# Performance work log

Hardware: AMD Instinct MI355X
Metric: run time of the kernel (lower is better)

The kernel has to match this reference:

```python
import jax, jax.numpy as jnp
import numpy as np

N, D, H1, K = 4096, 128, 256, 128


def setup_inputs() -> dict:
    key = jax.random.key(0)
    ks = jax.random.split(key, 8)
    A = jax.random.uniform(ks[3], (D, D), dtype=jnp.float32)
    A = A * (1.0 - jnp.eye(D, dtype=jnp.float32))  # DAG prob mask, no self-loops
    return {
        "x": jax.random.normal(ks[0], (N, D), dtype=jnp.float32),
        "weight": jax.random.normal(ks[1], (D, D), dtype=jnp.float32) * 0.1,
        "bias": jax.random.normal(ks[2], (1, D), dtype=jnp.float32) * 0.1,
        "A": A,
        "W1": jax.random.normal(ks[4], (D, H1), dtype=jnp.float32) * 0.1,
        "b1": jax.random.normal(ks[5], (H1,), dtype=jnp.float32) * 0.1,
        "W2": jax.random.normal(ks[6], (H1, K), dtype=jnp.float32) * 0.1,
        "b2": jax.random.normal(ks[7], (K,), dtype=jnp.float32) * 0.1,
    }


def reference(x, weight, bias, A, W1, b1, W2, b2):
    # to_adj (eval path): masked weights
    W = weight * A                                   # [D, D]
    y = x @ W + bias                                 # [N, D]
    # __expand__ builds diag(y[n]) [N,D,D]; since e[n,i,:] = y[n,i]*I[i,:],
    # the first Linear collapses to a per-row scaling of W1 (same math, fused):
    # e @ W1 -> y[n,i] * W1[i,:]
    h1 = jax.nn.relu(y[:, :, None] * W1[None, :, :] + b1)   # [N, D, H1]
    f = (h1 @ W2 + b2).sum(axis=2)                   # [N, D] (sum over output dim)
    # h_func, method='gnn'
    I = jnp.eye(D, dtype=x.dtype)
    A2 = jnp.square(W)
    M = I + A2 / D
    E = jnp.linalg.matrix_power(M, D - 1)
    h_val = (E.T * M).sum() - D
    # l1_reg (same prob mask in eval)
    reg = jnp.abs(W).sum()
    return (f, h_val, reg)
```

## Files before the change

### kernel.cpp

```cpp
#include <hip/hip_runtime.h>

#define NN 4096
#define DD 128
#define HH1 256

#define WS_S    0
#define WS_S2   16384
#define WS_S3   32768
#define WS_S4   49152
#define WS_W    65536
#define WS_W2S  81920
#define WS_PAIR 82176
#define WS_B2S  82688
#define WS_TACC 82696
#define WS_DONE 82708
#define WS_REGP 82712
#define WS_XT   82944
#define WS_REQ_FLOATS 607232
#define WS_REQ_BYTES  (WS_REQ_FLOATS * 4UL)

#define O_S    0
#define O_S2   16384
#define O_S3   32768
#define O_S4   49152
#define O_W2S  65536
#define O_B2S  65792
#define O_TACC 65808
#define O_DONE 65824
#define O_REGP 65840

__device__ __forceinline__ float waveReduce(float v) {
#pragma unroll
  for (int off = 32; off > 0; off >>= 1) v += __shfl_down(v, off, 64);
  return v;
}


__global__ __launch_bounds__(256) void kA2(
    const float* __restrict__ weight, const float* __restrict__ Amat,
    const float* __restrict__ W2, const float* __restrict__ b2,
    const float* __restrict__ b1v, const float* __restrict__ x,
    float* __restrict__ ws) {
  const int b = blockIdx.x, tid = threadIdx.x;
  __shared__ float s_lds[DD * DD];
  __shared__ float xs[128 * 133];
  if (b < 64) {
    const float4* w4 = (const float4*)weight;
    const float4* a4 = (const float4*)Amat;
    float4* s4 = (float4*)s_lds;
    const float inv = 1.0f / 128.0f;
    for (int e = tid; e < DD * DD / 4; e += 256) {
      float4 wv = w4[e], av = a4[e], o;
      float t;
      t = wv.x * av.x; o.x = t * t * inv;
      t = wv.y * av.y; o.y = t * t * inv;
      t = wv.z * av.z; o.z = t * t * inv;
      t = wv.w * av.w; o.w = t * t * inv;
      s4[e] = o;
    }
    __syncthreads();
    const int i = (b << 1) + (tid >> 7), j = tid & 127;
    const float* row = &s_lds[i * DD];
    float acc = 0.f;
#pragma unroll 8
    for (int k = 0; k < DD; ++k) acc = fmaf(row[k], s_lds[k * DD + j], acc);
    ws[WS_S2 + i * DD + j] = acc;
  } else if (b < 72) {
    const int base = (b - 64) * 2048;
    const float inv = 1.0f / 128.0f;
    for (int e = tid; e < 2048; e += 256) {
      const int idx = base + e;
      const float w = weight[idx] * Amat[idx];
      ws[WS_W + idx] = w;
      ws[WS_S + idx] = w * w * inv;
    }
  } else if (b == 72) {
    const float4* r = (const float4*)(W2 + tid * 128);
    float4 s4 = make_float4(0.f, 0.f, 0.f, 0.f);
#pragma unroll 8
    for (int k = 0; k < 32; ++k) {
      const float4 v = r[k];
      s4.x += v.x; s4.y += v.y; s4.z += v.z; s4.w += v.w;
    }
    const float w2sv = (s4.x + s4.y) + (s4.z + s4.w);
    ws[WS_W2S + tid] = w2sv;
    ((float2*)(ws + WS_PAIR))[tid] = make_float2(b1v[tid], w2sv);
  } else if (b == 73) {
    __shared__ float red[4];
    float v = (tid < 128) ? b2[tid] : 0.f;
    v = waveReduce(v);
    if ((tid & 63) == 0) red[tid >> 6] = v;
    __syncthreads();
    if (tid == 0) ws[WS_B2S] = (red[0] + red[1]) + (red[2] + red[3]);
    if (tid >= 64 && tid < 74) ws[WS_TACC + (tid - 64)] = 0.f;
    if (tid == 96) *(unsigned int*)(ws + WS_DONE) = 0u;
  } else if (b < 82) {
    const int bb = b - 74;
    const int base = bb * 2048;
    float s = 0.f;
    for (int e = tid; e < 2048; e += 256) {
      const int idx = base + e;
      s += fabsf(weight[idx] * Amat[idx]);
    }
    s = waveReduce(s);
    __shared__ float red2[4];
    if ((tid & 63) == 0) red2[tid >> 6] = s;
    __syncthreads();
    if (tid == 0) ws[WS_REGP + bb] = (red2[0] + red2[1]) + (red2[2] + red2[3]);
  } else {
    const int n0 = (b - 82) * 128;
    const float4* x4 = (const float4*)x;
    for (int e = tid; e < 4096; e += 256) {
      const int r = e >> 5, c = e & 31;
      const float4 v = x4[(n0 + r) * 32 + c];
      float* p = &xs[r * 133 + (c << 2)];
      p[0] = v.x; p[1] = v.y; p[2] = v.z; p[3] = v.w;
    }
    __syncthreads();
    float* xT = ws + WS_XT;
    const int c = tid & 31, ks = tid >> 5;
#pragma unroll 4
    for (int m = 0; m < 16; ++m) {
      const int k = ks + (m << 3);
      float4 o;
      o.x = xs[((c << 2) + 0) * 133 + k];
      o.y = xs[((c << 2) + 1) * 133 + k];
      o.z = xs[((c << 2) + 2) * 133 + k];
      o.w = xs[((c << 2) + 3) * 133 + k];
      *(float4*)&xT[k * NN + n0 + (c << 2)] = o;
    }
  }
}

__global__ __launch_bounds__(512) void kB3(const float* __restrict__ bias,
                                           const float* __restrict__ W1,
                                           float* __restrict__ ws,
                                           float* __restrict__ out) {
  const int tid = threadIdx.x;
  if (blockIdx.x < 64) {
    const int sb = blockIdx.x;
    const bool isS4 = sb >= 32;
    const int mb = isS4 ? sb - 32 : sb;
    const float* __restrict__ L = ws + WS_S2;
    const float* __restrict__ R = ws + (isS4 ? WS_S2 : WS_S);
    float* __restrict__ O = ws + (isS4 ? WS_S4 : WS_S3);
    const int i = (mb << 2) + (tid >> 7), j = tid & 127;
    float acc = 0.f;
#pragma unroll 8
    for (int k = 0; k < DD; ++k) acc = fmaf(L[i * DD + k], R[k * DD + j], acc);
    O[i * DD + j] = acc;
    return;
  }
  const int fb = blockIdx.x - 64;
  const int n0 = (fb & 15) << 8;
  const int i0 = (fb >> 4) << 3;
  const int w = tid >> 6, l = tid & 63;
  __shared__ float xs[32][256];
  __shared__ float ts[256][9];
  const float* __restrict__ xT = ws + WS_XT;
  const float* __restrict__ Wm = ws + WS_W;
  const int iu = __builtin_amdgcn_readfirstlane(i0 + w);

  float t[4] = {0.f, 0.f, 0.f, 0.f};
  for (int kc = 0; kc < 4; ++kc) {
    __syncthreads();
    {
      const float4* src = (const float4*)(xT + (kc * 32) * NN + n0);
      float4* dst4 = (float4*)&xs[0][0];
#pragma unroll
      for (int m = 0; m < 4; ++m) {
        const int e = tid + (m << 9);
        const int kk = e >> 6, c = e & 63;
        dst4[(kk << 6) + c] = src[kk * (NN / 4) + c];
      }
    }
    __syncthreads();
#pragma unroll
    for (int kk = 0; kk < 32; ++kk) {
      const float wv = Wm[(kc * 32 + kk) * DD + iu];
      const float4 xv = *(const float4*)&xs[kk][l << 2];
      t[0] = fmaf(xv.x, wv, t[0]);
      t[1] = fmaf(xv.y, wv, t[1]);
      t[2] = fmaf(xv.z, wv, t[2]);
      t[3] = fmaf(xv.w, wv, t[3]);
    }
  }
  const float bv = bias[iu];
#pragma unroll
  for (int q = 0; q < 4; ++q) t[q] += bv;

  const float sb2 = ws[WS_B2S];
  float acc[4];
#pragma unroll
  for (int q = 0; q < 4; ++q) acc[q] = sb2;
  const float* __restrict__ W1row = W1 + iu * HH1;
  const float2* __restrict__ pr = (const float2*)(ws + WS_PAIR);
#pragma unroll 8
  for (int j = 0; j < HH1; ++j) {
    const float sw1 = W1row[j];
    const float2 p = pr[j];
    const float vb = p.x;
#pragma unroll
    for (int q = 0; q < 4; ++q) {
      const float h = fmaxf(fmaf(t[q], sw1, vb), 0.f);
      acc[q] = fmaf(h, p.y, acc[q]);
    }
  }
#pragma unroll
  for (int q = 0; q < 4; ++q) ts[(l << 2) + q][w] = acc[q];
  __syncthreads();
  {
    const int m = tid >> 1, half = tid & 1;
    float4 o;
    o.x = ts[m][(half << 2) + 0];
    o.y = ts[m][(half << 2) + 1];
    o.z = ts[m][(half << 2) + 2];
    o.w = ts[m][(half << 2) + 3];
    *(float4*)&out[(n0 + m) * DD + i0 + (half << 2)] = o;
  }
}

__global__ __launch_bounds__(256) void kC3(float* __restrict__ ws,
                                           float* __restrict__ out) {
  const int tid = threadIdx.x;
  const int tb = blockIdx.x;
  const int i = (tb << 1) + (tid >> 7), j = tid & 127;
  const float* S1 = ws + WS_S;
  const float* S2 = ws + WS_S2;
  const float* S3 = ws + WS_S3;
  const float* S4 = ws + WS_S4;
  const float a1 = S1[i * DD + j], a2 = S2[i * DD + j], a3 = S3[i * DD + j];
  const float b1t = S1[j * DD + i], b2t = S2[j * DD + i],
              b3t = S3[j * DD + i], b4t = S4[j * DD + i];
  float e7 = 0.f;
#pragma unroll 8
  for (int k = 0; k < DD; ++k) e7 = fmaf(S3[i * DD + k], S4[k * DD + j], e7);
  float c[10];
  c[0] = a1 * b1t; c[1] = a2 * b1t; c[2] = a2 * b2t; c[3] = a3 * b2t;
  c[4] = a3 * b3t; c[5] = a3 * b4t; c[6] = e7 * b1t; c[7] = e7 * b2t;
  c[8] = e7 * b3t; c[9] = e7 * b4t;
  __shared__ float red[4][10];
#pragma unroll
  for (int m = 0; m < 10; ++m) {
    const float v = waveReduce(c[m]);
    if ((tid & 63) == 0) red[tid >> 6][m] = v;
  }
  __syncthreads();
  if (tid == 0) {
    float* tacc = ws + WS_TACC;
    for (int m = 0; m < 10; ++m)
      atomicAdd(&tacc[m], (red[0][m] + red[1][m]) + (red[2][m] + red[3][m]));
    __threadfence();
    unsigned int* done = (unsigned int*)(ws + WS_DONE);
    const unsigned int old = atomicAdd(done, 1u);
    if (old == 63u) {
      __threadfence();
      double h = 0.0, C = 8128.0;
      for (int kk = 2; kk <= 11; ++kk) {
        const float tv = atomicAdd(&tacc[kk - 2], 0.0f);
        h += C * (double)tv;
        C = C * (double)(128 - kk) / (double)(kk + 1);
      }
      float reg = 0.f;
      for (int m = 0; m < 8; ++m) reg += ws[WS_REGP + m];
      out[NN * DD] = (float)h;
      out[NN * DD + 1] = reg;
    }
  }
}

__global__ __launch_bounds__(256) void kA_old(
    const float* __restrict__ weight, const float* __restrict__ Amat,
    const float* __restrict__ W2, const float* __restrict__ b2,
    float* __restrict__ ws) {
  const int b = blockIdx.x, tid = threadIdx.x;
  if (b < 64) {
    __shared__ float s_lds[DD * DD];
    const float4* w4 = (const float4*)weight;
    const float4* a4 = (const float4*)Amat;
    float4* s4 = (float4*)s_lds;
    const float inv = 1.0f / 128.0f;
    for (int e = tid; e < DD * DD / 4; e += 256) {
      float4 wv = w4[e], av = a4[e], o;
      float t;
      t = wv.x * av.x; o.x = t * t * inv;
      t = wv.y * av.y; o.y = t * t * inv;
      t = wv.z * av.z; o.z = t * t * inv;
      t = wv.w * av.w; o.w = t * t * inv;
      s4[e] = o;
    }
    __syncthreads();
    const int i = (b << 1) + (tid >> 7), j = tid & 127;
    const float* row = &s_lds[i * DD];
    float acc = 0.f;
#pragma unroll 8
    for (int k = 0; k < DD; ++k) acc = fmaf(row[k], s_lds[k * DD + j], acc);
    ws[O_S2 + i * DD + j] = acc;
  } else if (b < 72) {
    const int base = (b - 64) * 2048;
    const float inv = 1.0f / 128.0f;
    for (int e = tid; e < 2048; e += 256) {
      const int idx = base + e;
      const float w = weight[idx] * Amat[idx];
      ws[O_S + idx] = w * w * inv;
    }
  } else if (b == 72) {
    const float4* r = (const float4*)(W2 + tid * 128);
    float4 s4 = make_float4(0.f, 0.f, 0.f, 0.f);
#pragma unroll 8
    for (int k = 0; k < 32; ++k) {
      const float4 v = r[k];
      s4.x += v.x; s4.y += v.y; s4.z += v.z; s4.w += v.w;
    }
    ws[O_W2S + tid] = (s4.x + s4.y) + (s4.z + s4.w);
  } else if (b == 73) {
    __shared__ float red[4];
    float v = (tid < 128) ? b2[tid] : 0.f;
    v = waveReduce(v);
    if ((tid & 63) == 0) red[tid >> 6] = v;
    __syncthreads();
    if (tid == 0) ws[O_B2S] = (red[0] + red[1]) + (red[2] + red[3]);
    if (tid >= 64 && tid < 74) ws[O_TACC + (tid - 64)] = 0.f;
    if (tid == 96) *(unsigned int*)(ws + O_DONE) = 0u;
  } else {
    const int bb = b - 74;
    const int base = bb * 2048;
    float s = 0.f;
    for (int e = tid; e < 2048; e += 256) {
      const int idx = base + e;
      s += fabsf(weight[idx] * Amat[idx]);
    }
    s = waveReduce(s);
    __shared__ float red[4];
    if ((tid & 63) == 0) red[tid >> 6] = s;
    __syncthreads();
    if (tid == 0) ws[O_REGP + bb] = (red[0] + red[1]) + (red[2] + red[3]);
  }
}

__global__ __launch_bounds__(256) void kB_old(
    const float* __restrict__ x, const float* __restrict__ weight,
    const float* __restrict__ Amat, const float* __restrict__ bias,
    const float* __restrict__ W1, const float* __restrict__ b1v,
    float* __restrict__ ws, float* __restrict__ out) {
  const int tid = threadIdx.x;
  if (blockIdx.x < 128) {
    const int sb = blockIdx.x;
    const bool isS4 = sb >= 64;
    const int mb = isS4 ? sb - 64 : sb;
    const float* __restrict__ L = ws + O_S2;
    const float* __restrict__ R = ws + (isS4 ? O_S2 : O_S);
    float* __restrict__ O = ws + (isS4 ? O_S4 : O_S3);
    const int i = (mb << 1) + (tid >> 7), j = tid & 127;
    float acc = 0.f;
#pragma unroll 8
    for (int k = 0; k < DD; ++k) acc = fmaf(L[i * DD + k], R[k * DD + j], acc);
    O[i * DD + j] = acc;
    return;
  }
  __shared__ float xs[64 * 132];
  __shared__ float4 fq[4 * 256];
  __shared__ float wcol[4 * 128];
  __shared__ float ts[64 * 5];
  const int fb = blockIdx.x - 128;
  const int i0 = (fb & 31) << 2, n0 = (fb >> 5) << 6;
  const float4* x4 = (const float4*)x;
  for (int e = tid; e < 64 * 32; e += 256) {
    const int r = e >> 5, c = e & 31;
    *(float4*)&xs[r * 132 + (c << 2)] = x4[(n0 + r) * 32 + c];
  }
  for (int e = tid; e < 512; e += 256) {
    const int w = e >> 7, k = e & 127;
    const int gi = k * DD + i0 + w;
    wcol[(w << 7) + k] = weight[gi] * Amat[gi];
  }
  const float* w2s = ws + O_W2S;
  for (int e = tid; e < 1024; e += 256) {
    const int w = e >> 8, j = e & 255;
    fq[(w << 8) + j] = make_float4(W1[(i0 + w) * HH1 + j], b1v[j], w2s[j], 0.f);
  }
  __syncthreads();
  const int w = tid >> 6, l = tid & 63;
  float t = bias[i0 + w];
  const float4* xr = (const float4*)&xs[l * 132];
  const float4* wc = (const float4*)&wcol[w << 7];
#pragma unroll
  for (int k = 0; k < 32; ++k) {
    const float4 xv = xr[k], wv = wc[k];
    t = fmaf(xv.x, wv.x, t);
    t = fmaf(xv.y, wv.y, t);
    t = fmaf(xv.z, wv.z, t);
    t = fmaf(xv.w, wv.w, t);
  }
  float acc = ws[O_B2S];
  const float4* fp = &fq[w << 8];
#pragma unroll 8
  for (int j = 0; j < HH1; ++j) {
    const float4 c = fp[j];
    acc = fmaf(fmaxf(fmaf(t, c.x, c.y), 0.f), c.z, acc);
  }
  ts[l * 5 + w] = acc;
  __syncthreads();
  if (tid < 64) {
    const float4 o = make_float4(ts[tid * 5 + 0], ts[tid * 5 + 1],
                                 ts[tid * 5 + 2], ts[tid * 5 + 3]);
    *(float4*)&out[(n0 + tid) * DD + i0] = o;
  }
}

__global__ __launch_bounds__(256) void kC_old(float* __restrict__ ws,
                                              float* __restrict__ out) {
  const int tid = threadIdx.x;
  const int i = (blockIdx.x << 1) + (tid >> 7), j = tid & 127;
  const float* S1 = ws + O_S;
  const float* S2 = ws + O_S2;
  const float* S3 = ws + O_S3;
  const float* S4 = ws + O_S4;
  const float a1 = S1[i * DD + j], a2 = S2[i * DD + j], a3 = S3[i * DD + j];
  const float b1t = S1[j * DD + i], b2t = S2[j * DD + i],
              b3t = S3[j * DD + i], b4t = S4[j * DD + i];
  float e7 = 0.f;
#pragma unroll 8
  for (int k = 0; k < DD; ++k) e7 = fmaf(S3[i * DD + k], S4[k * DD + j], e7);
  float c[10];
  c[0] = a1 * b1t; c[1] = a2 * b1t; c[2] = a2 * b2t; c[3] = a3 * b2t;
  c[4] = a3 * b3t; c[5] = a3 * b4t; c[6] = e7 * b1t; c[7] = e7 * b2t;
  c[8] = e7 * b3t; c[9] = e7 * b4t;
  __shared__ float red[4][10];
#pragma unroll
  for (int m = 0; m < 10; ++m) {
    const float v = waveReduce(c[m]);
    if ((tid & 63) == 0) red[tid >> 6][m] = v;
  }
  __syncthreads();
  if (tid == 0) {
    float* tacc = ws + O_TACC;
    for (int m = 0; m < 10; ++m)
      atomicAdd(&tacc[m], (red[0][m] + red[1][m]) + (red[2][m] + red[3][m]));
    __threadfence();
    unsigned int* done = (unsigned int*)(ws + O_DONE);
    const unsigned int old = atomicAdd(done, 1u);
    if (old == 63u) {
      __threadfence();
      double h = 0.0, C = 8128.0;
      for (int kk = 2; kk <= 11; ++kk) {
        const float tv = atomicAdd(&tacc[kk - 2], 0.0f);
        h += C * (double)tv;
        C = C * (double)(128 - kk) / (double)(kk + 1);
      }
      float reg = 0.f;
      for (int m = 0; m < 8; ++m) reg += ws[O_REGP + m];
      out[NN * DD] = (float)h;
      out[NN * DD + 1] = reg;
    }
  }
}

extern "C" void kernel_launch(void* const* d_in, const int* in_sizes, int n_in,
                              void* d_out, int out_size, void* d_ws,
                              size_t ws_size, hipStream_t stream) {
  const float* x      = (const float*)d_in[0];
  const float* weight = (const float*)d_in[1];
  const float* bias   = (const float*)d_in[2];
  const float* Amat   = (const float*)d_in[3];
  const float* W1     = (const float*)d_in[4];
  const float* b1v    = (const float*)d_in[5];
  const float* W2     = (const float*)d_in[6];
  const float* b2     = (const float*)d_in[7];
  float* out = (float*)d_out;
  float* ws  = (float*)d_ws;

  if (ws_size >= WS_REQ_BYTES) {
    kA2<<<114, 256, 0, stream>>>(weight, Amat, W2, b2, b1v, x, ws);
    kB3<<<320, 512, 0, stream>>>(bias, W1, ws, out);
    kC3<<<64, 256, 0, stream>>>(ws, out);
  } else {
    kA_old<<<82, 256, 0, stream>>>(weight, Amat, W2, b2, ws);
    kB_old<<<128 + 2048, 256, 0, stream>>>(x, weight, Amat, bias, W1, b1v, ws,
                                           out);
    kC_old<<<64, 256, 0, stream>>>(ws, out);
  }
}
```

Before: 116.3 us.

## Fuse three kernels into one persistent kernel with software grid barriers

```diff
diff --git a/kernel.cpp b/kernel.cpp
--- a/kernel.cpp
+++ b/kernel.cpp
@@ -15,8 +15,10 @@
 #define WS_TACC 82696
 #define WS_DONE 82708
 #define WS_REGP 82712
-#define WS_XT   82944
-#define WS_REQ_FLOATS 607232
+#define WS_BAR  82720
+#define WS_WT   82944
+#define WS_XT   99328
+#define WS_REQ_FLOATS 623616
 #define WS_REQ_BYTES  (WS_REQ_FLOATS * 4UL)
 
 #define O_S    0
@@ -35,21 +37,40 @@
   return v;
 }
 
-
-__global__ __launch_bounds__(256) void kA2(
-    const float* __restrict__ weight, const float* __restrict__ Amat,
+__device__ __forceinline__ void gridBarrier(unsigned int* bar,
+                                            unsigned int nblk) {
+  __syncthreads();
+  if (threadIdx.x == 0) {
+    __threadfence();
+    __hip_atomic_fetch_add(bar, 1u, __ATOMIC_ACQ_REL,
+                           __HIP_MEMORY_SCOPE_AGENT);
+    unsigned int v = __hip_atomic_load(bar, __ATOMIC_ACQUIRE,
+                                       __HIP_MEMORY_SCOPE_AGENT);
+    while (v < nblk) {
+      __builtin_amdgcn_s_sleep(2);
+      v = __hip_atomic_load(bar, __ATOMIC_ACQUIRE,
+                            __HIP_MEMORY_SCOPE_AGENT);
+    }
+  }
+  __syncthreads();
+}
+
+__global__ __launch_bounds__(512) void kFused(
+    const float* __restrict__ x, const float* __restrict__ weight,
+    const float* __restrict__ Amat, const float* __restrict__ bias,
+    const float* __restrict__ W1, const float* __restrict__ b1v,
     const float* __restrict__ W2, const float* __restrict__ b2,
-    const float* __restrict__ b1v, const float* __restrict__ x,
-    float* __restrict__ ws) {
+    float* __restrict__ ws, float* __restrict__ out) {
+  __shared__ float smem[17024];
   const int b = blockIdx.x, tid = threadIdx.x;
-  __shared__ float s_lds[DD * DD];
-  __shared__ float xs[128 * 133];
-  if (b < 64) {
+  unsigned int* bar = (unsigned int*)(ws + WS_BAR);
+
+  if (b < 32) {
     const float4* w4 = (const float4*)weight;
     const float4* a4 = (const float4*)Amat;
-    float4* s4 = (float4*)s_lds;
+    float4* s4 = (float4*)smem;
     const float inv = 1.0f / 128.0f;
-    for (int e = tid; e < DD * DD / 4; e += 256) {
+    for (int e = tid; e < DD * DD / 4; e += 512) {
       float4 wv = w4[e], av = a4[e], o;
       float t;
       t = wv.x * av.x; o.x = t * t * inv;
@@ -59,88 +80,165 @@
       s4[e] = o;
     }
     __syncthreads();
-    const int i = (b << 1) + (tid >> 7), j = tid & 127;
-    const float* row = &s_lds[i * DD];
+    const int i = (b << 2) + (tid >> 7), j = tid & 127;
+    const float* row = &smem[i * DD];
     float acc = 0.f;
 #pragma unroll 8
-    for (int k = 0; k < DD; ++k) acc = fmaf(row[k], s_lds[k * DD + j], acc);
+    for (int k = 0; k < DD; ++k) acc = fmaf(row[k], smem[k * DD + j], acc);
     ws[WS_S2 + i * DD + j] = acc;
-  } else if (b < 72) {
-    const int base = (b - 64) * 2048;
+  } else if (b < 40) {
+    const int base = (b - 32) * 2048;
     const float inv = 1.0f / 128.0f;
-    for (int e = tid; e < 2048; e += 256) {
+    for (int e = tid; e < 2048; e += 512) {
       const int idx = base + e;
       const float w = weight[idx] * Amat[idx];
+      const int k = idx >> 7, i = idx & 127;
       ws[WS_W + idx] = w;
+      ws[WS_WT + i * DD + k] = w;
       ws[WS_S + idx] = w * w * inv;
     }
-  } else if (b == 72) {
-    const float4* r = (const float4*)(W2 + tid * 128);
-    float4 s4 = make_float4(0.f, 0.f, 0.f, 0.f);
-#pragma unroll 8
-    for (int k = 0; k < 32; ++k) {
-      const float4 v = r[k];
-      s4.x += v.x; s4.y += v.y; s4.z += v.z; s4.w += v.w;
-    }
-    const float w2sv = (s4.x + s4.y) + (s4.z + s4.w);
-    ws[WS_W2S + tid] = w2sv;
-    ((float2*)(ws + WS_PAIR))[tid] = make_float2(b1v[tid], w2sv);
-  } else if (b == 73) {
-    __shared__ float red[4];
+  } else if (b == 40) {
+    if (tid < 256) {
+      const float4* r = (const float4*)(W2 + tid * 128);
+      float4 s4 = make_float4(0.f, 0.f, 0.f, 0.f);
+#pragma unroll 8
+      for (int k = 0; k < 32; ++k) {
+        const float4 v = r[k];
+        s4.x += v.x; s4.y += v.y; s4.z += v.z; s4.w += v.w;
+      }
+      const float w2sv = (s4.x + s4.y) + (s4.z + s4.w);
+      ws[WS_W2S + tid] = w2sv;
+      ((float2*)(ws + WS_PAIR))[tid] = make_float2(b1v[tid], w2sv);
+    }
+  } else if (b == 41) {
     float v = (tid < 128) ? b2[tid] : 0.f;
     v = waveReduce(v);
+    float* red = smem;
     if ((tid & 63) == 0) red[tid >> 6] = v;
     __syncthreads();
-    if (tid == 0) ws[WS_B2S] = (red[0] + red[1]) + (red[2] + red[3]);
+    if (tid == 0) {
+      float s = 0.f;
+      for (int m = 0; m < 8; ++m) s += red[m];
+      ws[WS_B2S] = s;
+    }
     if (tid >= 64 && tid < 74) ws[WS_TACC + (tid - 64)] = 0.f;
     if (tid == 96) *(unsigned int*)(ws + WS_DONE) = 0u;
-  } else if (b < 82) {
-    const int bb = b - 74;
+  } else if (b < 50) {
+    const int bb = b - 42;
     const int base = bb * 2048;
     float s = 0.f;
-    for (int e = tid; e < 2048; e += 256) {
+    for (int e = tid; e < 2048; e += 512) {
       const int idx = base + e;
       s += fabsf(weight[idx] * Amat[idx]);
     }
     s = waveReduce(s);
-    __shared__ float red2[4];
+    float* red2 = smem;
     if ((tid & 63) == 0) red2[tid >> 6] = s;
     __syncthreads();
-    if (tid == 0) ws[WS_REGP + bb] = (red2[0] + red2[1]) + (red2[2] + red2[3]);
-  } else {
-    const int n0 = (b - 82) * 128;
+    if (tid == 0) {
+      float t = 0.f;
+      for (int m = 0; m < 8; ++m) t += red2[m];
+      ws[WS_REGP + bb] = t;
+    }
+  } else if (b < 82) {
+    const int n0 = (b - 50) * 128;
     const float4* x4 = (const float4*)x;
-    for (int e = tid; e < 4096; e += 256) {
+    for (int e = tid; e < 4096; e += 512) {
       const int r = e >> 5, c = e & 31;
       const float4 v = x4[(n0 + r) * 32 + c];
-      float* p = &xs[r * 133 + (c << 2)];
+      float* p = &smem[r * 133 + (c << 2)];
       p[0] = v.x; p[1] = v.y; p[2] = v.z; p[3] = v.w;
     }
     __syncthreads();
     float* xT = ws + WS_XT;
     const int c = tid & 31, ks = tid >> 5;
-#pragma unroll 4
-    for (int m = 0; m < 16; ++m) {
-      const int k = ks + (m << 3);
+#pragma unroll
+    for (int m = 0; m < 8; ++m) {
+      const int k = ks + (m << 4);
       float4 o;
-      o.x = xs[((c << 2) + 0) * 133 + k];
-      o.y = xs[((c << 2) + 1) * 133 + k];
-      o.z = xs[((c << 2) + 2) * 133 + k];
-      o.w = xs[((c << 2) + 3) * 133 + k];
+      o.x = smem[((c << 2) + 0) * 133 + k];
+      o.y = smem[((c << 2) + 1) * 133 + k];
+      o.z = smem[((c << 2) + 2) * 133 + k];
+      o.w = smem[((c << 2) + 3) * 133 + k];
       *(float4*)&xT[k * NN + n0 + (c << 2)] = o;
     }
   }
-}
-
-__global__ __launch_bounds__(512) void kB3(const float* __restrict__ bias,
-                                           const float* __restrict__ W1,
-                                           float* __restrict__ ws,
-                                           float* __restrict__ out) {
-  const int tid = threadIdx.x;
-  if (blockIdx.x < 64) {
-    const int sb = blockIdx.x;
-    const bool isS4 = sb >= 32;
-    const int mb = isS4 ? sb - 32 : sb;
+
+  gridBarrier(bar, 256);
+
+  {
+    const int fb = b;
+    const int n0 = (fb & 15) << 8, i0 = (fb >> 4) << 3;
+    const int w = tid >> 6, l = tid & 63;
+    float* xs = smem;
+    float* ts = smem + 8192;
+    const float* __restrict__ xT = ws + WS_XT;
+    const float* __restrict__ WTm = ws + WS_WT;
+    const int iu = __builtin_amdgcn_readfirstlane(i0 + w);
+
+    float t[4] = {0.f, 0.f, 0.f, 0.f};
+    for (int kc = 0; kc < 4; ++kc) {
+      __syncthreads();
+      {
+        const float4* src = (const float4*)(xT + (kc * 32) * NN + n0);
+        float4* dst4 = (float4*)xs;
+#pragma unroll
+        for (int m = 0; m < 4; ++m) {
+          const int e = tid + (m << 9);
+          const int kk = e >> 6, c = e & 63;
+          dst4[(kk << 6) + c] = src[kk * (NN / 4) + c];
+        }
+      }
+      __syncthreads();
+      const float* wr = WTm + iu * DD + kc * 32;
+#pragma unroll
+      for (int kk = 0; kk < 32; ++kk) {
+        const float wv = wr[kk];
+        const float4 xv = *(const float4*)&xs[kk * 256 + (l << 2)];
+        t[0] = fmaf(xv.x, wv, t[0]);
+        t[1] = fmaf(xv.y, wv, t[1]);
+        t[2] = fmaf(xv.z, wv, t[2]);
+        t[3] = fmaf(xv.w, wv, t[3]);
+      }
+    }
+    const float bv = bias[iu];
+#pragma unroll
+    for (int q = 0; q < 4; ++q) t[q] += bv;
+
+    const float sb2 = ws[WS_B2S];
+    float acc[4];
+#pragma unroll
+    for (int q = 0; q < 4; ++q) acc[q] = sb2;
+    const float* __restrict__ W1row = W1 + iu * HH1;
+    const float2* __restrict__ pr = (const float2*)(ws + WS_PAIR);
+#pragma unroll 8
+    for (int j = 0; j < HH1; ++j) {
+      const float sw1 = W1row[j];
+      const float2 p = pr[j];
+      const float vb = p.x;
+#pragma unroll
+      for (int q = 0; q < 4; ++q) {
+        const float h = fmaxf(fmaf(t[q], sw1, vb), 0.f);
+        acc[q] = fmaf(h, p.y, acc[q]);
+      }
+    }
+#pragma unroll
+    for (int q = 0; q < 4; ++q) ts[((l << 2) + q) * 9 + w] = acc[q];
+    __syncthreads();
+    {
+      const int m = tid >> 1, half = tid & 1;
+      float4 o;
+      o.x = ts[m * 9 + (half << 2) + 0];
+      o.y = ts[m * 9 + (half << 2) + 1];
+      o.z = ts[m * 9 + (half << 2) + 2];
+      o.w = ts[m * 9 + (half << 2) + 3];
+      *(float4*)&out[(n0 + m) * DD + i0 + (half << 2)] = o;
+    }
+  }
+
+  if (b < 64) {
+    const bool isS4 = b >= 32;
+    const int mb = b & 31;
     const float* __restrict__ L = ws + WS_S2;
     const float* __restrict__ R = ws + (isS4 ? WS_S2 : WS_S);
     float* __restrict__ O = ws + (isS4 ? WS_S4 : WS_S3);
@@ -149,122 +247,58 @@
 #pragma unroll 8
     for (int k = 0; k < DD; ++k) acc = fmaf(L[i * DD + k], R[k * DD + j], acc);
     O[i * DD + j] = acc;
-    return;
-  }
-  const int fb = blockIdx.x - 64;
-  const int n0 = (fb & 15) << 8;
-  const int i0 = (fb >> 4) << 3;
-  const int w = tid >> 6, l = tid & 63;
-  __shared__ float xs[32][256];
-  __shared__ float ts[256][9];
-  const float* __restrict__ xT = ws + WS_XT;
-  const float* __restrict__ Wm = ws + WS_W;
-  const int iu = __builtin_amdgcn_readfirstlane(i0 + w);
-
-  float t[4] = {0.f, 0.f, 0.f, 0.f};
-  for (int kc = 0; kc < 4; ++kc) {
-    __syncthreads();
-    {
-      const float4* src = (const float4*)(xT + (kc * 32) * NN + n0);
-      float4* dst4 = (float4*)&xs[0][0];
-#pragma unroll
-      for (int m = 0; m < 4; ++m) {
-        const int e = tid + (m << 9);
-        const int kk = e >> 6, c = e & 63;
-        dst4[(kk << 6) + c] = src[kk * (NN / 4) + c];
-      }
-    }
-    __syncthreads();
-#pragma unroll
-    for (int kk = 0; kk < 32; ++kk) {
-      const float wv = Wm[(kc * 32 + kk) * DD + iu];
-      const float4 xv = *(const float4*)&xs[kk][l << 2];
-      t[0] = fmaf(xv.x, wv, t[0]);
-      t[1] = fmaf(xv.y, wv, t[1]);
-      t[2] = fmaf(xv.z, wv, t[2]);
-      t[3] = fmaf(xv.w, wv, t[3]);
-    }
-  }
-  const float bv = bias[iu];
-#pragma unroll
-  for (int q = 0; q < 4; ++q) t[q] += bv;
-
-  const float sb2 = ws[WS_B2S];
-  float acc[4];
-#pragma unroll
-  for (int q = 0; q < 4; ++q) acc[q] = sb2;
-  const float* __restrict__ W1row = W1 + iu * HH1;
-  const float2* __restrict__ pr = (const float2*)(ws + WS_PAIR);
-#pragma unroll 8
-  for (int j = 0; j < HH1; ++j) {
-    const float sw1 = W1row[j];
-    const float2 p = pr[j];
-    const float vb = p.x;
-#pragma unroll
-    for (int q = 0; q < 4; ++q) {
-      const float h = fmaxf(fmaf(t[q], sw1, vb), 0.f);
-      acc[q] = fmaf(h, p.y, acc[q]);
-    }
-  }
-#pragma unroll
-  for (int q = 0; q < 4; ++q) ts[(l << 2) + q][w] = acc[q];
-  __syncthreads();
+  }
+
+  gridBarrier(bar + 1, 256);
+
+  if (b >= 32) return;
+
   {
-    const int m = tid >> 1, half = tid & 1;
-    float4 o;
-    o.x = ts[m][(half << 2) + 0];
-    o.y = ts[m][(half << 2) + 1];
-    o.z = ts[m][(half << 2) + 2];
-    o.w = ts[m][(half << 2) + 3];
-    *(float4*)&out[(n0 + m) * DD + i0 + (half << 2)] = o;
-  }
-}
-
-__global__ __launch_bounds__(256) void kC3(float* __restrict__ ws,
-                                           float* __restrict__ out) {
-  const int tid = threadIdx.x;
-  const int tb = blockIdx.x;
-  const int i = (tb << 1) + (tid >> 7), j = tid & 127;
-  const float* S1 = ws + WS_S;
-  const float* S2 = ws + WS_S2;
-  const float* S3 = ws + WS_S3;
-  const float* S4 = ws + WS_S4;
-  const float a1 = S1[i * DD + j], a2 = S2[i * DD + j], a3 = S3[i * DD + j];
-  const float b1t = S1[j * DD + i], b2t = S2[j * DD + i],
-              b3t = S3[j * DD + i], b4t = S4[j * DD + i];
-  float e7 = 0.f;
-#pragma unroll 8
-  for (int k = 0; k < DD; ++k) e7 = fmaf(S3[i * DD + k], S4[k * DD + j], e7);
-  float c[10];
-  c[0] = a1 * b1t; c[1] = a2 * b1t; c[2] = a2 * b2t; c[3] = a3 * b2t;
-  c[4] = a3 * b3t; c[5] = a3 * b4t; c[6] = e7 * b1t; c[7] = e7 * b2t;
-  c[8] = e7 * b3t; c[9] = e7 * b4t;
-  __shared__ float red[4][10];
-#pragma unroll
-  for (int m = 0; m < 10; ++m) {
-    const float v = waveReduce(c[m]);
-    if ((tid & 63) == 0) red[tid >> 6][m] = v;
-  }
-  __syncthreads();
-  if (tid == 0) {
-    float* tacc = ws + WS_TACC;
-    for (int m = 0; m < 10; ++m)
-      atomicAdd(&tacc[m], (red[0][m] + red[1][m]) + (red[2][m] + red[3][m]));
-    __threadfence();
-    unsigned int* done = (unsigned int*)(ws + WS_DONE);
-    const unsigned int old = atomicAdd(done, 1u);
-    if (old == 63u) {
+    const int i = (b << 2) + (tid >> 7), j = tid & 127;
+    const float* S1 = ws + WS_S;
+    const float* S2 = ws + WS_S2;
+    const float* S3 = ws + WS_S3;
+    const float* S4 = ws + WS_S4;
+    const float a1 = S1[i * DD + j], a2 = S2[i * DD + j], a3 = S3[i * DD + j];
+    const float b1t = S1[j * DD + i], b2t = S2[j * DD + i],
+                b3t = S3[j * DD + i], b4t = S4[j * DD + i];
+    float e7 = 0.f;
+#pragma unroll 8
+    for (int k = 0; k < DD; ++k) e7 = fmaf(S3[i * DD + k], S4[k * DD + j], e7);
+    float c[10];
+    c[0] = a1 * b1t; c[1] = a2 * b1t; c[2] = a2 * b2t; c[3] = a3 * b2t;
+    c[4] = a3 * b3t; c[5] = a3 * b4t; c[6] = e7 * b1t; c[7] = e7 * b2t;
+    c[8] = e7 * b3t; c[9] = e7 * b4t;
+    float* red = smem;
+#pragma unroll
+    for (int m = 0; m < 10; ++m) {
+      const float v = waveReduce(c[m]);
+      if ((tid & 63) == 0) red[(tid >> 6) * 10 + m] = v;
+    }
+    __syncthreads();
+    if (tid == 0) {
+      float* tacc = ws + WS_TACC;
+      for (int m = 0; m < 10; ++m) {
+        float s = 0.f;
+        for (int wv = 0; wv < 8; ++wv) s += red[wv * 10 + m];
+        atomicAdd(&tacc[m], s);
+      }
       __threadfence();
-      double h = 0.0, C = 8128.0;
-      for (int kk = 2; kk <= 11; ++kk) {
-        const float tv = atomicAdd(&tacc[kk - 2], 0.0f);
-        h += C * (double)tv;
-        C = C * (double)(128 - kk) / (double)(kk + 1);
-      }
-      float reg = 0.f;
-      for (int m = 0; m < 8; ++m) reg += ws[WS_REGP + m];
-      out[NN * DD] = (float)h;
-      out[NN * DD + 1] = reg;
+      unsigned int* done = (unsigned int*)(ws + WS_DONE);
+      const unsigned int old = atomicAdd(done, 1u);
+      if (old == 31u) {
+        __threadfence();
+        double h = 0.0, C = 8128.0;
+        for (int kk = 2; kk <= 11; ++kk) {
+          const float tv = atomicAdd(&tacc[kk - 2], 0.0f);
+          h += C * (double)tv;
+          C = C * (double)(128 - kk) / (double)(kk + 1);
+        }
+        float reg = 0.f;
+        for (int m = 0; m < 8; ++m) reg += ws[WS_REGP + m];
+        out[NN * DD] = (float)h;
+        out[NN * DD + 1] = reg;
+      }
     }
   }
 }
@@ -471,9 +505,9 @@
   float* ws  = (float*)d_ws;
 
   if (ws_size >= WS_REQ_BYTES) {
-    kA2<<<114, 256, 0, stream>>>(weight, Amat, W2, b2, b1v, x, ws);
-    kB3<<<320, 512, 0, stream>>>(bias, W1, ws, out);
-    kC3<<<64, 256, 0, stream>>>(ws, out);
+    hipMemsetAsync((char*)d_ws + WS_BAR * 4UL, 0, 16, stream);
+    kFused<<<256, 512, 0, stream>>>(x, weight, Amat, bias, W1, b1v, W2, b2,
+                                    ws, out);
   } else {
     kA_old<<<82, 256, 0, stream>>>(weight, Amat, W2, b2, ws);
     kB_old<<<128 + 2048, 256, 0, stream>>>(x, weight, Amat, bias, W1, b1v, ws,
```

New measurement: 198.2 us. 1.7x slower.
